# Optimization experiments

Measured on AMD Instinct MI355X. Metric: run time of the kernel, lower is better.

## Reference

```python
import jax, jax.numpy as jnp
import numpy as np

B, D, O = 512, 256, 128  # batch, input_dim, output_dim


def setup_inputs() -> dict:
    key = jax.random.key(0)
    k1, k2, k3, k4, k5, k6 = jax.random.split(key, 6)
    eyeD = jnp.eye(D, dtype=jnp.float32)
    # density-like inputs: diagonal offset keeps the trace denominator well-conditioned
    x_real = jax.random.normal(k1, (B, D, D), dtype=jnp.float32) + 2.0 * eyeD
    x_imag = jax.random.normal(k2, (B, D, D), dtype=jnp.float32)
    # weight = identity + small perturbation (module inits to [eye, zeros] stacked)
    w_r = eyeD + 0.02 * jax.random.normal(k3, (D, D), dtype=jnp.float32)
    w_i = 0.02 * jax.random.normal(k4, (D, D), dtype=jnp.float32)
    weight = jnp.stack([w_r, w_i], axis=-1)  # [D, D, 2]
    rand_w = jax.random.uniform(k5, (O,), dtype=jnp.float32)
    lam = jax.random.uniform(k6, (1,), dtype=jnp.float32)
    return {"x_real": x_real, "x_imag": x_imag, "weight": weight,
            "rand_w": rand_w, "lam": lam}


def reference(x_real, x_imag, weight, rand_w, lam):
    out_dim = rand_w.shape[0]
    U_r = weight[:, :, 0]  # [D, D]
    U_i = weight[:, :, 1]
    # evolution: (U_r + i U_i) X (U_r + i U_i)^H, batched over b
    R = jnp.einsum('ij,bjk->bik', U_r, x_real) - jnp.einsum('ij,bjk->bik', U_i, x_imag)
    I = jnp.einsum('ij,bjk->bik', U_i, x_real) + jnp.einsum('ij,bjk->bik', U_r, x_imag)
    out_r = jnp.einsum('bik,jk->bij', R, U_r) + jnp.einsum('bik,jk->bij', I, U_i)
    out_i = jnp.einsum('bik,jk->bij', I, U_r) - jnp.einsum('bik,jk->bij', R, U_i)
    # input_dim >= output_dim branch: top-left block, normalized by trace of real part
    sub_r = out_r[:, :out_dim, :out_dim]
    sub_i = out_i[:, :out_dim, :out_dim]
    tr = jnp.trace(sub_r, axis1=1, axis2=2)[:, None, None]  # [B,1,1]
    norm_r = sub_r / tr
    norm_i = sub_i / tr
    p = jax.nn.softmax(rand_w, axis=-1)
    s = jax.nn.sigmoid(lam[0])
    output_r = s * norm_r + (1.0 - s) * jnp.diag(p)
    output_i = s * norm_i
    return (output_r, output_i)
```

## Files before the change

kernel.cpp:

```cpp
#include <hip/hip_runtime.h>
#include <hip/hip_bf16.h>


typedef __attribute__((ext_vector_type(4))) float f32x4;
typedef __attribute__((ext_vector_type(8))) short bf16x8;

static __device__ __forceinline__ short f2bf(float f) {
    unsigned u = __float_as_uint(f);
    u += 0x7fffu + ((u >> 16) & 1u);
    return (short)(u >> 16);
}

static __device__ __forceinline__ float b2f(unsigned short h) {
    return __uint_as_float(((unsigned)h) << 16);
}

static __device__ __forceinline__ unsigned cvtpk2(float lo, float hi) {
    union { __hip_bfloat162 h; unsigned u; } c;
    c.h = __float22bfloat162_rn(float2{lo, hi});
    return c.u;
}

static __device__ __forceinline__ uint2 cvt2(f32x4 v) {
    uint2 r;
    r.x = cvtpk2(v[0], v[1]);
    r.y = cvtpk2(v[2], v[3]);
    return r;
}

static __device__ __forceinline__ f32x4 mfma16(bf16x8 a, bf16x8 b, f32x4 c) {
    return __builtin_amdgcn_mfma_f32_16x16x32_bf16(a, b, c, 0, 0, 0);
}

__global__ void qprep_u(const float* __restrict__ wt,
                        short* __restrict__ Ur,  short* __restrict__ Ui,
                        short* __restrict__ Upr, short* __restrict__ Upi) {
    int idx = blockIdx.x * 256 + threadIdx.x;
    int j = idx >> 8, k = idx & 255;
    float2 v = ((const float2*)wt)[idx];
    short br = f2bf(v.x), bi = f2bf(v.y);
    Ur[idx] = br;
    Ui[idx] = bi;
    int g = j >> 4, s = k >> 5;
    int lanep = (j & 15) | (((k >> 3) & 3) << 4);
    int p = ((g * 8 + s) * 64 + lanep) * 8 + (k & 7);
    Upr[p] = br;
    Upi[p] = bi;
}

__global__ void qprep_ps(const float* __restrict__ rw, const float* __restrict__ lm,
                         float* __restrict__ pv, float* __restrict__ sv) {
    int t = threadIdx.x;
    float w0 = rw[t], w1 = rw[t + 64];
    float m = fmaxf(w0, w1);
    #pragma unroll
    for (int o = 32; o > 0; o >>= 1) m = fmaxf(m, __shfl_xor(m, o));
    float e0 = expf(w0 - m), e1 = expf(w1 - m);
    float ss = e0 + e1;
    #pragma unroll
    for (int o = 32; o > 0; o >>= 1) ss += __shfl_xor(ss, o);
    pv[t] = e0 / ss;
    pv[t + 64] = e1 / ss;
    if (t == 0) sv[0] = 1.f / (1.f + expf(-lm[0]));
}

__global__ void qprep_q(const float* __restrict__ wt,
                        short* __restrict__ Qrb, short* __restrict__ Qib) {
    int j = blockIdx.x;
    int k = threadIdx.x;
    float ar = 0.f, ai = 0.f;
    for (int i = 0; i < 128; ++i) {
        float2 uk = ((const float2*)wt)[i * 256 + k];
        float2 uj = ((const float2*)wt)[i * 256 + j];
        ar += uk.x * uj.x + uk.y * uj.y;
        ai += uk.x * uj.y - uk.y * uj.x;
    }
    Qrb[j * 256 + k] = f2bf(ar);
    Qib[j * 256 + k] = f2bf(ai);
}

#define PB(Q) ((Q) * 32)

#define TRDOT(RB, A0, A1, A2, A3) do {                                          \
    const int qo0 = ((RB) + sr0) * 256 + xl4;                                   \
    const int qo1 = ((RB) + sr1) * 256 + xl4;                                   \
    ushort4 hr0 = *(const ushort4*)(Qrb + qo0);                                 \
    ushort4 hr1 = *(const ushort4*)(Qrb + qo1);                                 \
    ushort4 hi0 = *(const ushort4*)(Qib + qo0);                                 \
    ushort4 hi1 = *(const ushort4*)(Qib + qo1);                                 \
    tracc += A0[0]*b2f(hr0.x) + A0[1]*b2f(hr0.y)                                \
           + A0[2]*b2f(hr0.z) + A0[3]*b2f(hr0.w);                               \
    tracc += A1[0]*b2f(hr1.x) + A1[1]*b2f(hr1.y)                                \
           + A1[2]*b2f(hr1.z) + A1[3]*b2f(hr1.w);                               \
    tracc -= A2[0]*b2f(hi0.x) + A2[1]*b2f(hi0.y)                                \
           + A2[2]*b2f(hi0.z) + A2[3]*b2f(hi0.w);                               \
    tracc -= A3[0]*b2f(hi1.x) + A3[1]*b2f(hi1.y)                                \
           + A3[2]*b2f(hi1.z) + A3[3]*b2f(hi1.w);                               \
} while (0)

#define CONS(KS) do {                                                           \
    const int ko = (KS) * 64 + g16;                                             \
    bf16x8 axr = *(const bf16x8*)(xsp + aro + (ko ^ aswz));                     \
    bf16x8 axi = *(const bf16x8*)(xsp + 8192 + aro + (ko ^ aswz));              \
    bf16x8 bur = *(const bf16x8*)(smem + uob + (ko ^ uswz));                    \
    bf16x8 bui = *(const bf16x8*)(smem + 32768 + uob + (ko ^ uswz));            \
    bf16x8 axrn = axr ^ (short)0x8000;                                          \
    yR = mfma16(axr,  bur, yR);                                                 \
    yR = mfma16(axi,  bui, yR);                                                 \
    yI = mfma16(axi,  bur, yI);                                                 \
    yI = mfma16(axrn, bui, yI);                                                 \
} while (0)

#define PAIR(Q) do {                                                            \
    const char* xsp = smem + 81920 + ((Q) & 1) * 32768 + wj16k;                 \
    if ((Q) < 7) {     \
        char* wp0 = smem + 81920 + (((Q) + 1) & 1) * 32768;                     \
        *(uint2*)(wp0 + wr0o)        = cvt2(hA0);                               \
        *(uint2*)(wp0 + wr1o)        = cvt2(hA1);                               \
        *(uint2*)(wp0 + 8192 + wr0o) = cvt2(hA2);                               \
        *(uint2*)(wp0 + 8192 + wr1o) = cvt2(hA3);                               \
        TRDOT(PB((Q) + 1), hA0, hA1, hA2, hA3);                                 \
        const int r0 = (PB((Q) + 1) + 16 + sr0) * 256 + xl4;                    \
        const int r1 = (PB((Q) + 1) + 16 + sr1) * 256 + xl4;                    \
        hA0 = *(const f32x4*)(xr + xgb + r0);     \
        hA1 = *(const f32x4*)(xr + xgb + r1);                                   \
        hA2 = *(const f32x4*)(xi + xgb + r0);                                   \
        hA3 = *(const f32x4*)(xi + xgb + r1);                                   \
    }                                                                           \
    __builtin_amdgcn_sched_barrier(0);                                          \
    CONS(0); CONS(1); CONS(2); CONS(3);                                         \
    if ((Q) < 7) {                           \
        char* wp1 = smem + 81920 + (((Q) + 1) & 1) * 32768 + 16384;             \
        *(uint2*)(wp1 + wr0o)        = cvt2(hA0);                               \
        *(uint2*)(wp1 + wr1o)        = cvt2(hA1);                               \
        *(uint2*)(wp1 + 8192 + wr0o) = cvt2(hA2);                               \
        *(uint2*)(wp1 + 8192 + wr1o) = cvt2(hA3);                               \
        TRDOT(PB((Q) + 1) + 16, hA0, hA1, hA2, hA3);                            \
    }                                                                           \
    if ((Q) < 6) {                                \
        const int r0 = (PB((Q) + 2) + sr0) * 256 + xl4;                         \
        const int r1 = (PB((Q) + 2) + sr1) * 256 + xl4;                         \
        hA0 = *(const f32x4*)(xr + xgb + r0);                                   \
        hA1 = *(const f32x4*)(xr + xgb + r1);                                   \
        hA2 = *(const f32x4*)(xi + xgb + r0);                                   \
        hA3 = *(const f32x4*)(xi + xgb + r1);                                   \
    }                                                                           \
    __builtin_amdgcn_sched_barrier(0);                                          \
    CONS(4); CONS(5); CONS(6); CONS(7);                                         \
    {                                                                           \
        const int yw = ((Q) & 1) ? ytw1 : ytw0;                                 \
        *(uint2*)(smem + 65536 + yw) = cvt2(yR);                                \
        *(uint2*)(smem + 73728 + yw) = cvt2(yI);                                \
    }                                                                           \
    yR = zero; yI = zero;                                                       \
    asm volatile("s_waitcnt lgkmcnt(0)" ::: "memory");                          \
    __builtin_amdgcn_sched_barrier(0);                                          \
    __builtin_amdgcn_s_barrier();                                               \
    __builtin_amdgcn_sched_barrier(0);                                          \
} while (0)

#define STAGEB_KS(JT, KS2) do {                                                 \
    const int s2 = (JT) * 2 + (KS2);                                            \
    bf16x8 aur0 = *(const bf16x8*)(Upr + ((wm * 2 + 0) * 8 + s2) * 512 + l8);   \
    bf16x8 aui0 = *(const bf16x8*)(Upi + ((wm * 2 + 0) * 8 + s2) * 512 + l8);   \
    bf16x8 aur1 = *(const bf16x8*)(Upr + ((wm * 2 + 1) * 8 + s2) * 512 + l8);   \
    bf16x8 aui1 = *(const bf16x8*)(Upi + ((wm * 2 + 1) * 8 + s2) * 512 + l8);   \
    bf16x8 auin0 = aui0 ^ (short)0x8000;                                        \
    bf16x8 auin1 = aui1 ^ (short)0x8000;                                        \
    {                                                                           \
        const int off = ybA + (((KS2) * 64 + g16) ^ ysA);                       \
        bf16x8 byr = *(const bf16x8*)(smem + 65536 + off);                      \
        bf16x8 byi = *(const bf16x8*)(smem + 73728 + off);                      \
        sR00 = mfma16(aur0,  byr, sR00); sR00 = mfma16(auin0, byi, sR00);       \
        sI00 = mfma16(aui0,  byr, sI00); sI00 = mfma16(aur0,  byi, sI00);       \
        sR10 = mfma16(aur1,  byr, sR10); sR10 = mfma16(auin1, byi, sR10);       \
        sI10 = mfma16(aui1,  byr, sI10); sI10 = mfma16(aur1,  byi, sI10);       \
    }                                                                           \
    {                                                                           \
        const int off = ybB + (((KS2) * 64 + g16) ^ ysB);                       \
        bf16x8 byr = *(const bf16x8*)(smem + 65536 + off);                      \
        bf16x8 byi = *(const bf16x8*)(smem + 73728 + off);                      \
        sR01 = mfma16(aur0,  byr, sR01); sR01 = mfma16(auin0, byi, sR01);       \
        sI01 = mfma16(aui0,  byr, sI01); sI01 = mfma16(aur0,  byi, sI01);       \
        sR11 = mfma16(aur1,  byr, sR11); sR11 = mfma16(auin1, byi, sR11);       \
        sI11 = mfma16(aui1,  byr, sI11); sI11 = mfma16(aur1,  byi, sI11);       \
    }                                                                           \
} while (0)

#define STAGEB_PASS(JT) do {                                                    \
    STAGEB_KS(JT, 0);                                                           \
    STAGEB_KS(JT, 1);                                                           \
    asm volatile("s_waitcnt lgkmcnt(0)" ::: "memory");                          \
    __builtin_amdgcn_sched_barrier(0);                                          \
    __builtin_amdgcn_s_barrier();         \
    __builtin_amdgcn_sched_barrier(0);                                          \
} while (0)

__global__ __launch_bounds__(512, 1) void qfused(
    const float* __restrict__ xr, const float* __restrict__ xi,
    const short* __restrict__ Urg, const short* __restrict__ Uig,
    const short* __restrict__ Upr, const short* __restrict__ Upi,
    const short* __restrict__ Qrb, const short* __restrict__ Qib,
    const float* __restrict__ pv, const float* __restrict__ sv,
    float* __restrict__ out)
{
    __shared__ __align__(16) char smem[147456];

    const int bx   = blockIdx.x;
    const int b    = ((bx >> 4) << 3) | (bx & 7);
    const int kh   = (bx >> 3) & 1;
    const int tid  = threadIdx.x;
    const int lane = tid & 63;
    const int w    = tid >> 6;
    const int c16  = lane & 15;
    const int g4   = lane >> 4;
    const int g8   = g4 * 8;
    const int g16  = g4 * 16;
    const int l8   = lane * 8;

    const int wj    = w >> 2;
    const int wk    = w & 3;
    const int wj16k = wj * 16384;
    const int wm    = w >> 1;
    const int wn    = w & 1;

    const int sr0 = w * 2, sr1 = w * 2 + 1;
    const int xl4 = lane * 4;
    const int xgb = b << 16;
    const int wr0o = sr0 * 512 + ((((lane >> 1) << 4) ^ ((sr0 & 7) << 4))) + ((lane & 1) << 3);
    const int wr1o = sr1 * 512 + ((((lane >> 1) << 4) ^ ((sr1 & 7) << 4))) + ((lane & 1) << 3);

    const int aro  = c16 * 512;
    const int aswz = (c16 & 7) << 4;
    const int ukl  = wk * 16 + c16;
    const int uob  = ukl * 512;
    const int uswz = (ukl & 7) << 4;

    const int ytr  = ukl;
    const int ytk  = (ytr & 7) << 4;
    const int ytw0 = ytr * 128 + ((wj * 32 + g8) ^ ytk);
    const int ytw1 = ytr * 128 + ((64 + wj * 32 + g8) ^ ytk);

    const int ybA = (wn * 32 + c16) * 128;
    const int ybB = (wn * 32 + 16 + c16) * 128;
    const int ysA = ((wn * 32 + c16) & 7) << 4;
    const int ysB = ((wn * 32 + 16 + c16) & 7) << 4;

    #pragma unroll
    for (int q = 0; q < 4; ++q) {
        int c    = tid + q * 512;
        int row  = c >> 5;
        int slot = c & 31;
        int ss   = slot ^ (row & 7);
        const short* sr = Urg + (size_t)(kh * 64 + row) * 256 + ss * 8;
        const short* si = Uig + (size_t)(kh * 64 + row) * 256 + ss * 8;
        *(bf16x8*)(smem + row * 512 + slot * 16)         = *(const bf16x8*)sr;
        *(bf16x8*)(smem + 32768 + row * 512 + slot * 16) = *(const bf16x8*)si;
    }

    f32x4 zero = {0.f, 0.f, 0.f, 0.f};
    f32x4 sR00 = zero, sR01 = zero, sR10 = zero, sR11 = zero;
    f32x4 sI00 = zero, sI01 = zero, sI10 = zero, sI11 = zero;
    float tracc = 0.f;
    f32x4 yR = zero, yI = zero;
    f32x4 hA0, hA1, hA2, hA3;

    {
        const int r0 = (PB(0) + sr0) * 256 + xl4;
        const int r1 = (PB(0) + sr1) * 256 + xl4;
        const int r2 = (PB(0) + 16 + sr0) * 256 + xl4;
        const int r3 = (PB(0) + 16 + sr1) * 256 + xl4;
        f32x4 a0 = *(const f32x4*)(xr + xgb + r0);
        f32x4 a1 = *(const f32x4*)(xr + xgb + r1);
        f32x4 a2 = *(const f32x4*)(xi + xgb + r0);
        f32x4 a3 = *(const f32x4*)(xi + xgb + r1);
        f32x4 b0 = *(const f32x4*)(xr + xgb + r2);
        f32x4 b1 = *(const f32x4*)(xr + xgb + r3);
        f32x4 b2 = *(const f32x4*)(xi + xgb + r2);
        f32x4 b3 = *(const f32x4*)(xi + xgb + r3);
        const int r4 = (PB(1) + sr0) * 256 + xl4;
        const int r5 = (PB(1) + sr1) * 256 + xl4;
        hA0 = *(const f32x4*)(xr + xgb + r4);
        hA1 = *(const f32x4*)(xr + xgb + r5);
        hA2 = *(const f32x4*)(xi + xgb + r4);
        hA3 = *(const f32x4*)(xi + xgb + r5);
        char* w0p = smem + 81920;
        char* w1p = smem + 81920 + 16384;
        *(uint2*)(w0p + wr0o)        = cvt2(a0);
        *(uint2*)(w0p + wr1o)        = cvt2(a1);
        *(uint2*)(w0p + 8192 + wr0o) = cvt2(a2);
        *(uint2*)(w0p + 8192 + wr1o) = cvt2(a3);
        *(uint2*)(w1p + wr0o)        = cvt2(b0);
        *(uint2*)(w1p + wr1o)        = cvt2(b1);
        *(uint2*)(w1p + 8192 + wr0o) = cvt2(b2);
        *(uint2*)(w1p + 8192 + wr1o) = cvt2(b3);
        TRDOT(PB(0),      a0, a1, a2, a3);
        TRDOT(PB(0) + 16, b0, b1, b2, b3);
    }
    asm volatile("s_waitcnt lgkmcnt(0)" ::: "memory");
    __builtin_amdgcn_sched_barrier(0);
    __builtin_amdgcn_s_barrier();
    __builtin_amdgcn_sched_barrier(0);

    PAIR(0);
    PAIR(1);
    STAGEB_PASS(0);
    PAIR(2);
    PAIR(3);
    STAGEB_PASS(1);
    PAIR(4);
    PAIR(5);
    STAGEB_PASS(2);
    PAIR(6);
    PAIR(7);
    STAGEB_KS(3, 0);
    STAGEB_KS(3, 1);

    float loc = tracc;
    #pragma unroll
    for (int o = 32; o > 0; o >>= 1) loc += __shfl_xor(loc, o);
    __syncthreads();
    float* red = (float*)(smem + 65536);
    if (lane == 0) red[w] = loc;
    __syncthreads();
    float tr = red[0] + red[1] + red[2] + red[3] +
               red[4] + red[5] + red[6] + red[7];

    float s     = sv[0];
    float inv   = s / tr;
    float onems = 1.f - s;
    float* outr = out + (size_t)b * 16384;
    float* outi = out + 8388608 + (size_t)b * 16384;

    #define EPI(SRV, SIV, MT, NT) do {                                          \
        int colc = kh * 64 + wn * 32 + (NT) * 16 + c16;                         \
        _Pragma("unroll")                                                       \
        for (int r = 0; r < 4; ++r) {                                           \
            int row = wm * 32 + (MT) * 16 + g4 * 4 + r;                         \
            float vr = SRV[r] * inv;                                            \
            if (row == colc) vr += onems * pv[row];                             \
            outr[row * 128 + colc] = vr;                                        \
            outi[row * 128 + colc] = SIV[r] * inv;                              \
        }                                                                       \
    } while (0)

    EPI(sR00, sI00, 0, 0);
    EPI(sR01, sI01, 0, 1);
    EPI(sR10, sI10, 1, 0);
    EPI(sR11, sI11, 1, 1);
    #undef EPI
}

extern "C" void kernel_launch(void* const* d_in, const int* in_sizes, int n_in,
                              void* d_out, int out_size, void* d_ws, size_t ws_size,
                              hipStream_t stream) {
    (void)in_sizes; (void)n_in; (void)out_size; (void)ws_size;
    const float* xr = (const float*)d_in[0];
    const float* xi = (const float*)d_in[1];
    const float* wt = (const float*)d_in[2];
    const float* rw = (const float*)d_in[3];
    const float* lm = (const float*)d_in[4];

    short* Ur  = (short*)d_ws;
    short* Ui  = (short*)((char*)d_ws + 65536);
    short* Upr = (short*)((char*)d_ws + 131072);
    short* Upi = (short*)((char*)d_ws + 196608);
    short* Qrb = (short*)((char*)d_ws + 262144);
    short* Qib = (short*)((char*)d_ws + 393216);
    float* pv  = (float*)((char*)d_ws + 524288);
    float* sv  = pv + 128;
    float* o   = (float*)d_out;

    qprep_u<<<dim3(128), dim3(256), 0, stream>>>(wt, Ur, Ui, Upr, Upi);
    qprep_ps<<<dim3(1), dim3(64), 0, stream>>>(rw, lm, pv, sv);
    qprep_q<<<dim3(256), dim3(256), 0, stream>>>(wt, Qrb, Qib);
    qfused<<<dim3(1024), dim3(512), 0, stream>>>(xr, xi, Ur, Ui, Upr, Upi,
                                                 Qrb, Qib, pv, sv, o);
}
```

Baseline: 148.1 us.

## Prefetch trace weights with x rows and stage epilogue through LDS for vector stores

The Q trace-weight loads are now issued together with the prefetch of the next x rows into held registers, so the trace dot product no longer waits on fresh global loads. The epilogue writes results into padded shared memory and then issues coalesced 16-byte global stores instead of scattered scalar stores. Y-tile addressing is simplified by XORing the offset, and the reduction buffer moves to an unused shared-memory region. This uses more registers and adds a barrier plus an LDS round trip in the epilogue.

```diff
diff --git a/kernel.cpp b/kernel.cpp
--- a/kernel.cpp
+++ b/kernel.cpp
@@ -81,7 +81,7 @@
 
 #define PB(Q) ((Q) * 32)
 
-#define TRDOT(RB, A0, A1, A2, A3) do {                                          \
+#define TRDOT_DIR(RB, A0, A1, A2, A3) do {                                      \
     const int qo0 = ((RB) + sr0) * 256 + xl4;                                   \
     const int qo1 = ((RB) + sr1) * 256 + xl4;                                   \
     ushort4 hr0 = *(const ushort4*)(Qrb + qo0);                                 \
@@ -98,6 +98,17 @@
            + A3[2]*b2f(hi1.z) + A3[3]*b2f(hi1.w);                               \
 } while (0)
 
+#define TRDOT_HELD() do {                                                       \
+    tracc += hA0[0]*b2f(hq0.x) + hA0[1]*b2f(hq0.y)                              \
+           + hA0[2]*b2f(hq0.z) + hA0[3]*b2f(hq0.w);                             \
+    tracc += hA1[0]*b2f(hq1.x) + hA1[1]*b2f(hq1.y)                              \
+           + hA1[2]*b2f(hq1.z) + hA1[3]*b2f(hq1.w);                             \
+    tracc -= hA2[0]*b2f(hq2.x) + hA2[1]*b2f(hq2.y)                              \
+           + hA2[2]*b2f(hq2.z) + hA2[3]*b2f(hq2.w);                             \
+    tracc -= hA3[0]*b2f(hq3.x) + hA3[1]*b2f(hq3.y)                              \
+           + hA3[2]*b2f(hq3.z) + hA3[3]*b2f(hq3.w);                             \
+} while (0)
+
 #define CONS(KS) do {                                                           \
     const int ko = (KS) * 64 + g16;                                             \
     bf16x8 axr = *(const bf16x8*)(xsp + aro + (ko ^ aswz));                     \
@@ -113,42 +124,50 @@
 
 #define PAIR(Q) do {                                                            \
     const char* xsp = smem + 81920 + ((Q) & 1) * 32768 + wj16k;                 \
-    if ((Q) < 7) {     \
+    if ((Q) < 7) {       \
         char* wp0 = smem + 81920 + (((Q) + 1) & 1) * 32768;                     \
         *(uint2*)(wp0 + wr0o)        = cvt2(hA0);                               \
         *(uint2*)(wp0 + wr1o)        = cvt2(hA1);                               \
         *(uint2*)(wp0 + 8192 + wr0o) = cvt2(hA2);                               \
         *(uint2*)(wp0 + 8192 + wr1o) = cvt2(hA3);                               \
-        TRDOT(PB((Q) + 1), hA0, hA1, hA2, hA3);                                 \
+        TRDOT_HELD();                                                           \
         const int r0 = (PB((Q) + 1) + 16 + sr0) * 256 + xl4;                    \
         const int r1 = (PB((Q) + 1) + 16 + sr1) * 256 + xl4;                    \
         hA0 = *(const f32x4*)(xr + xgb + r0);     \
         hA1 = *(const f32x4*)(xr + xgb + r1);                                   \
         hA2 = *(const f32x4*)(xi + xgb + r0);                                   \
         hA3 = *(const f32x4*)(xi + xgb + r1);                                   \
+        hq0 = *(const ushort4*)(Qrb + r0);                                      \
+        hq1 = *(const ushort4*)(Qrb + r1);                                      \
+        hq2 = *(const ushort4*)(Qib + r0);                                      \
+        hq3 = *(const ushort4*)(Qib + r1);                                      \
     }                                                                           \
     __builtin_amdgcn_sched_barrier(0);                                          \
     CONS(0); CONS(1); CONS(2); CONS(3);                                         \
-    if ((Q) < 7) {                           \
+    if ((Q) < 7) {                 \
         char* wp1 = smem + 81920 + (((Q) + 1) & 1) * 32768 + 16384;             \
         *(uint2*)(wp1 + wr0o)        = cvt2(hA0);                               \
         *(uint2*)(wp1 + wr1o)        = cvt2(hA1);                               \
         *(uint2*)(wp1 + 8192 + wr0o) = cvt2(hA2);                               \
         *(uint2*)(wp1 + 8192 + wr1o) = cvt2(hA3);                               \
-        TRDOT(PB((Q) + 1) + 16, hA0, hA1, hA2, hA3);                            \
-    }                                                                           \
-    if ((Q) < 6) {                                \
+        TRDOT_HELD();                                                           \
+    }                                                                           \
+    if ((Q) < 6) {                             \
         const int r0 = (PB((Q) + 2) + sr0) * 256 + xl4;                         \
         const int r1 = (PB((Q) + 2) + sr1) * 256 + xl4;                         \
         hA0 = *(const f32x4*)(xr + xgb + r0);                                   \
         hA1 = *(const f32x4*)(xr + xgb + r1);                                   \
         hA2 = *(const f32x4*)(xi + xgb + r0);                                   \
         hA3 = *(const f32x4*)(xi + xgb + r1);                                   \
+        hq0 = *(const ushort4*)(Qrb + r0);                                      \
+        hq1 = *(const ushort4*)(Qrb + r1);                                      \
+        hq2 = *(const ushort4*)(Qib + r0);                                      \
+        hq3 = *(const ushort4*)(Qib + r1);                                      \
     }                                                                           \
     __builtin_amdgcn_sched_barrier(0);                                          \
     CONS(4); CONS(5); CONS(6); CONS(7);                                         \
     {                                                                           \
-        const int yw = ((Q) & 1) ? ytw1 : ytw0;                                 \
+        const int yw = ytw0 ^ (((Q) & 1) << 6);                                 \
         *(uint2*)(smem + 65536 + yw) = cvt2(yR);                                \
         *(uint2*)(smem + 73728 + yw) = cvt2(yI);                                \
     }                                                                           \
@@ -177,7 +196,7 @@
         sI10 = mfma16(aui1,  byr, sI10); sI10 = mfma16(aur1,  byi, sI10);       \
     }                                                                           \
     {                                                                           \
-        const int off = ybB + (((KS2) * 64 + g16) ^ ysB);                       \
+        const int off = ybA + 2048 + (((KS2) * 64 + g16) ^ ysA);                \
         bf16x8 byr = *(const bf16x8*)(smem + 65536 + off);                      \
         bf16x8 byi = *(const bf16x8*)(smem + 73728 + off);                      \
         sR01 = mfma16(aur0,  byr, sR01); sR01 = mfma16(auin0, byi, sR01);       \
@@ -236,15 +255,10 @@
     const int uob  = ukl * 512;
     const int uswz = (ukl & 7) << 4;
 
-    const int ytr  = ukl;
-    const int ytk  = (ytr & 7) << 4;
-    const int ytw0 = ytr * 128 + ((wj * 32 + g8) ^ ytk);
-    const int ytw1 = ytr * 128 + ((64 + wj * 32 + g8) ^ ytk);
+    const int ytw0 = ukl * 128 + ((wj * 32 + g8) ^ ((ukl & 7) << 4));
 
     const int ybA = (wn * 32 + c16) * 128;
-    const int ybB = (wn * 32 + 16 + c16) * 128;
     const int ysA = ((wn * 32 + c16) & 7) << 4;
-    const int ysB = ((wn * 32 + 16 + c16) & 7) << 4;
 
     #pragma unroll
     for (int q = 0; q < 4; ++q) {
@@ -264,6 +278,7 @@
     float tracc = 0.f;
     f32x4 yR = zero, yI = zero;
     f32x4 hA0, hA1, hA2, hA3;
+    ushort4 hq0, hq1, hq2, hq3;
 
     {
         const int r0 = (PB(0) + sr0) * 256 + xl4;
@@ -284,6 +299,10 @@
         hA1 = *(const f32x4*)(xr + xgb + r5);
         hA2 = *(const f32x4*)(xi + xgb + r4);
         hA3 = *(const f32x4*)(xi + xgb + r5);
+        hq0 = *(const ushort4*)(Qrb + r4);
+        hq1 = *(const ushort4*)(Qrb + r5);
+        hq2 = *(const ushort4*)(Qib + r4);
+        hq3 = *(const ushort4*)(Qib + r5);
         char* w0p = smem + 81920;
         char* w1p = smem + 81920 + 16384;
         *(uint2*)(w0p + wr0o)        = cvt2(a0);
@@ -294,8 +313,8 @@
         *(uint2*)(w1p + wr1o)        = cvt2(b1);
         *(uint2*)(w1p + 8192 + wr0o) = cvt2(b2);
         *(uint2*)(w1p + 8192 + wr1o) = cvt2(b3);
-        TRDOT(PB(0),      a0, a1, a2, a3);
-        TRDOT(PB(0) + 16, b0, b1, b2, b3);
+        TRDOT_DIR(PB(0),      a0, a1, a2, a3);
+        TRDOT_DIR(PB(0) + 16, b0, b1, b2, b3);
     }
     asm volatile("s_waitcnt lgkmcnt(0)" ::: "memory");
     __builtin_amdgcn_sched_barrier(0);
@@ -320,7 +339,7 @@
     #pragma unroll
     for (int o = 32; o > 0; o >>= 1) loc += __shfl_xor(loc, o);
     __syncthreads();
-    float* red = (float*)(smem + 65536);
+    float* red = (float*)(smem + 143360);
     if (lane == 0) red[w] = loc;
     __syncthreads();
     float tr = red[0] + red[1] + red[2] + red[3] +
@@ -329,26 +348,40 @@
     float s     = sv[0];
     float inv   = s / tr;
     float onems = 1.f - s;
-    float* outr = out + (size_t)b * 16384;
-    float* outi = out + 8388608 + (size_t)b * 16384;
-
-    #define EPI(SRV, SIV, MT, NT) do {                                          \
-        int colc = kh * 64 + wn * 32 + (NT) * 16 + c16;                         \
+
+    float* smfR = (float*)smem;
+    float* smfI = (float*)(smem + 81920);
+
+    #define EPW(SRV, SIV, MT, NT) do {                                          \
+        int colc = wn * 32 + (NT) * 16 + c16;              \
         _Pragma("unroll")                                                       \
         for (int r = 0; r < 4; ++r) {                                           \
             int row = wm * 32 + (MT) * 16 + g4 * 4 + r;                         \
             float vr = SRV[r] * inv;                                            \
-            if (row == colc) vr += onems * pv[row];                             \
-            outr[row * 128 + colc] = vr;                                        \
-            outi[row * 128 + colc] = SIV[r] * inv;                              \
+            if (row == kh * 64 + colc) vr += onems * pv[row];                   \
+            smfR[row * 68 + colc] = vr;                                         \
+            smfI[row * 68 + colc] = SIV[r] * inv;                               \
         }                                                                       \
     } while (0)
 
-    EPI(sR00, sI00, 0, 0);
-    EPI(sR01, sI01, 0, 1);
-    EPI(sR10, sI10, 1, 0);
-    EPI(sR11, sI11, 1, 1);
-    #undef EPI
+    EPW(sR00, sI00, 0, 0);
+    EPW(sR01, sI01, 0, 1);
+    EPW(sR10, sI10, 1, 0);
+    EPW(sR11, sI11, 1, 1);
+    #undef EPW
+    __syncthreads();
+
+    float* outr = out + (size_t)b * 16384 + kh * 64;
+    float* outi = out + 8388608 + (size_t)b * 16384 + kh * 64;
+    #pragma unroll
+    for (int it = 0; it < 4; ++it) {
+        int rowl = w * 16 + it * 4 + (lane >> 4);
+        int colL = c16 * 4;
+        f32x4 vR = *(const f32x4*)(smfR + rowl * 68 + colL);
+        f32x4 vI = *(const f32x4*)(smfI + rowl * 68 + colL);
+        *(f32x4*)(outr + (size_t)rowl * 128 + colL) = vR;
+        *(f32x4*)(outi + (size_t)rowl * 128 + colL) = vI;
+    }
 }
 
 extern "C" void kernel_launch(void* const* d_in, const int* in_sizes, int n_in,
```

New measurement: 151.6 us. +2.4%, slower.

## Stream pre-packed U fragments from global memory instead of staging U in LDS

Applied to the files above, without the earlier changes.

The first-stage MFMA B operands (U real/imag) are now loaded directly from the pre-packed fragment layout in global memory, one k-step ahead in registers, instead of copying U into a 64KB LDS region at kernel start. This drops the row-major U copies from the prep kernel and shrinks shared memory from 144KB to 80KB, and the X staging buffers move to offset zero. The intent is to remove the LDS fill, its bank traffic and the startup latency. The cost is more global/L2 loads inside the inner MFMA loop, and their latency may not be fully hidden by one-step prefetching. Occupancy is likely unchanged because of launch_bounds(512,1).

```diff
diff --git a/kernel.cpp b/kernel.cpp
--- a/kernel.cpp
+++ b/kernel.cpp
@@ -33,19 +33,15 @@
 }
 
 __global__ void qprep_u(const float* __restrict__ wt,
-                        short* __restrict__ Ur,  short* __restrict__ Ui,
                         short* __restrict__ Upr, short* __restrict__ Upi) {
     int idx = blockIdx.x * 256 + threadIdx.x;
     int j = idx >> 8, k = idx & 255;
     float2 v = ((const float2*)wt)[idx];
-    short br = f2bf(v.x), bi = f2bf(v.y);
-    Ur[idx] = br;
-    Ui[idx] = bi;
     int g = j >> 4, s = k >> 5;
     int lanep = (j & 15) | (((k >> 3) & 3) << 4);
     int p = ((g * 8 + s) * 64 + lanep) * 8 + (k & 7);
-    Upr[p] = br;
-    Upi[p] = bi;
+    Upr[p] = f2bf(v.x);
+    Upi[p] = f2bf(v.y);
 }
 
 __global__ void qprep_ps(const float* __restrict__ rw, const float* __restrict__ lm,
@@ -102,8 +98,9 @@
     const int ko = (KS) * 64 + g16;                                             \
     bf16x8 axr = *(const bf16x8*)(xsp + aro + (ko ^ aswz));                     \
     bf16x8 axi = *(const bf16x8*)(xsp + 8192 + aro + (ko ^ aswz));              \
-    bf16x8 bur = *(const bf16x8*)(smem + uob + (ko ^ uswz));                    \
-    bf16x8 bui = *(const bf16x8*)(smem + 32768 + uob + (ko ^ uswz));            \
+    bf16x8 bur = uhr, bui = uhi;                                                \
+    uhr = *(const bf16x8*)(Upr + ubA + ((((KS) + 1) & 7) << 9));                \
+    uhi = *(const bf16x8*)(Upi + ubA + ((((KS) + 1) & 7) << 9));                \
     bf16x8 axrn = axr ^ (short)0x8000;                                          \
     yR = mfma16(axr,  bur, yR);                                                 \
     yR = mfma16(axi,  bui, yR);                                                 \
@@ -112,9 +109,9 @@
 } while (0)
 
 #define PAIR(Q) do {                                                            \
-    const char* xsp = smem + 81920 + ((Q) & 1) * 32768 + wj16k;                 \
+    const char* xsp = smem + ((Q) & 1) * 32768 + wj16k;                         \
     if ((Q) < 7) {     \
-        char* wp0 = smem + 81920 + (((Q) + 1) & 1) * 32768;                     \
+        char* wp0 = smem + (((Q) + 1) & 1) * 32768;                             \
         *(uint2*)(wp0 + wr0o)        = cvt2(hA0);                               \
         *(uint2*)(wp0 + wr1o)        = cvt2(hA1);                               \
         *(uint2*)(wp0 + 8192 + wr0o) = cvt2(hA2);                               \
@@ -130,7 +127,7 @@
     __builtin_amdgcn_sched_barrier(0);                                          \
     CONS(0); CONS(1); CONS(2); CONS(3);                                         \
     if ((Q) < 7) {                           \
-        char* wp1 = smem + 81920 + (((Q) + 1) & 1) * 32768 + 16384;             \
+        char* wp1 = smem + (((Q) + 1) & 1) * 32768 + 16384;                     \
         *(uint2*)(wp1 + wr0o)        = cvt2(hA0);                               \
         *(uint2*)(wp1 + wr1o)        = cvt2(hA1);                               \
         *(uint2*)(wp1 + 8192 + wr0o) = cvt2(hA2);                               \
@@ -148,7 +145,7 @@
     __builtin_amdgcn_sched_barrier(0);                                          \
     CONS(4); CONS(5); CONS(6); CONS(7);                                         \
     {                                                                           \
-        const int yw = ((Q) & 1) ? ytw1 : ytw0;                                 \
+        const int yw = ytw0 ^ (((Q) & 1) << 6);                                 \
         *(uint2*)(smem + 65536 + yw) = cvt2(yR);                                \
         *(uint2*)(smem + 73728 + yw) = cvt2(yI);                                \
     }                                                                           \
@@ -177,7 +174,7 @@
         sI10 = mfma16(aui1,  byr, sI10); sI10 = mfma16(aur1,  byi, sI10);       \
     }                                                                           \
     {                                                                           \
-        const int off = ybB + (((KS2) * 64 + g16) ^ ysB);                       \
+        const int off = ybA + 2048 + (((KS2) * 64 + g16) ^ ysA);                \
         bf16x8 byr = *(const bf16x8*)(smem + 65536 + off);                      \
         bf16x8 byi = *(const bf16x8*)(smem + 73728 + off);                      \
         sR01 = mfma16(aur0,  byr, sR01); sR01 = mfma16(auin0, byi, sR01);       \
@@ -198,13 +195,12 @@
 
 __global__ __launch_bounds__(512, 1) void qfused(
     const float* __restrict__ xr, const float* __restrict__ xi,
-    const short* __restrict__ Urg, const short* __restrict__ Uig,
     const short* __restrict__ Upr, const short* __restrict__ Upi,
     const short* __restrict__ Qrb, const short* __restrict__ Qib,
     const float* __restrict__ pv, const float* __restrict__ sv,
     float* __restrict__ out)
 {
-    __shared__ __align__(16) char smem[147456];
+    __shared__ __align__(16) char smem[81920];
 
     const int bx   = blockIdx.x;
     const int b    = ((bx >> 4) << 3) | (bx & 7);
@@ -232,31 +228,13 @@
 
     const int aro  = c16 * 512;
     const int aswz = (c16 & 7) << 4;
+    const int ubA  = (kh * 4 + wk) * 4096 + l8;
+
     const int ukl  = wk * 16 + c16;
-    const int uob  = ukl * 512;
-    const int uswz = (ukl & 7) << 4;
-
-    const int ytr  = ukl;
-    const int ytk  = (ytr & 7) << 4;
-    const int ytw0 = ytr * 128 + ((wj * 32 + g8) ^ ytk);
-    const int ytw1 = ytr * 128 + ((64 + wj * 32 + g8) ^ ytk);
+    const int ytw0 = ukl * 128 + ((wj * 32 + g8) ^ ((ukl & 7) << 4));
 
     const int ybA = (wn * 32 + c16) * 128;
-    const int ybB = (wn * 32 + 16 + c16) * 128;
     const int ysA = ((wn * 32 + c16) & 7) << 4;
-    const int ysB = ((wn * 32 + 16 + c16) & 7) << 4;
-
-    #pragma unroll
-    for (int q = 0; q < 4; ++q) {
-        int c    = tid + q * 512;
-        int row  = c >> 5;
-        int slot = c & 31;
-        int ss   = slot ^ (row & 7);
-        const short* sr = Urg + (size_t)(kh * 64 + row) * 256 + ss * 8;
-        const short* si = Uig + (size_t)(kh * 64 + row) * 256 + ss * 8;
-        *(bf16x8*)(smem + row * 512 + slot * 16)         = *(const bf16x8*)sr;
-        *(bf16x8*)(smem + 32768 + row * 512 + slot * 16) = *(const bf16x8*)si;
-    }
 
     f32x4 zero = {0.f, 0.f, 0.f, 0.f};
     f32x4 sR00 = zero, sR01 = zero, sR10 = zero, sR11 = zero;
@@ -264,6 +242,7 @@
     float tracc = 0.f;
     f32x4 yR = zero, yI = zero;
     f32x4 hA0, hA1, hA2, hA3;
+    bf16x8 uhr, uhi;
 
     {
         const int r0 = (PB(0) + sr0) * 256 + xl4;
@@ -284,8 +263,10 @@
         hA1 = *(const f32x4*)(xr + xgb + r5);
         hA2 = *(const f32x4*)(xi + xgb + r4);
         hA3 = *(const f32x4*)(xi + xgb + r5);
-        char* w0p = smem + 81920;
-        char* w1p = smem + 81920 + 16384;
+        uhr = *(const bf16x8*)(Upr + ubA);
+        uhi = *(const bf16x8*)(Upi + ubA);
+        char* w0p = smem;
+        char* w1p = smem + 16384;
         *(uint2*)(w0p + wr0o)        = cvt2(a0);
         *(uint2*)(w0p + wr1o)        = cvt2(a1);
         *(uint2*)(w0p + 8192 + wr0o) = cvt2(a2);
@@ -361,19 +342,17 @@
     const float* rw = (const float*)d_in[3];
     const float* lm = (const float*)d_in[4];
 
-    short* Ur  = (short*)d_ws;
-    short* Ui  = (short*)((char*)d_ws + 65536);
-    short* Upr = (short*)((char*)d_ws + 131072);
-    short* Upi = (short*)((char*)d_ws + 196608);
-    short* Qrb = (short*)((char*)d_ws + 262144);
-    short* Qib = (short*)((char*)d_ws + 393216);
-    float* pv  = (float*)((char*)d_ws + 524288);
+    short* Upr = (short*)d_ws;
+    short* Upi = (short*)((char*)d_ws + 65536);
+    short* Qrb = (short*)((char*)d_ws + 131072);
+    short* Qib = (short*)((char*)d_ws + 262144);
+    float* pv  = (float*)((char*)d_ws + 393216);
     float* sv  = pv + 128;
     float* o   = (float*)d_out;
 
-    qprep_u<<<dim3(128), dim3(256), 0, stream>>>(wt, Ur, Ui, Upr, Upi);
+    qprep_u<<<dim3(128), dim3(256), 0, stream>>>(wt, Upr, Upi);
     qprep_ps<<<dim3(1), dim3(64), 0, stream>>>(rw, lm, pv, sv);
     qprep_q<<<dim3(256), dim3(256), 0, stream>>>(wt, Qrb, Qib);
-    qfused<<<dim3(1024), dim3(512), 0, stream>>>(xr, xi, Ur, Ui, Upr, Upi,
+    qfused<<<dim3(1024), dim3(512), 0, stream>>>(xr, xi, Upr, Upi,
                                                  Qrb, Qib, pv, sv, o);
 }
```

Measured after the change: 165.0 us. 11.4% more time.
